# Kernel tuning notes

Hardware: AMD Instinct MI355X
Metric: run time of the kernel (lower is better)

Reference implementation:

```python
import jax, jax.numpy as jnp
import numpy as np

EMBED_DIM = 1024
NUM_HEADS = 16
D_K = EMBED_DIM // NUM_HEADS
MAX_SEQ = 2048
BATCH = 2
SEQ = 2048
ROPE_BASE = 10000.0


def build_rope(seq_len, head_dim, base=ROPE_BASE):
    # standard RoPE: inv_freq over half the head dim, cos/sin of shape [seq, head_dim]
    inv_freq = 1.0 / (base ** (jnp.arange(0, head_dim, 2, dtype=jnp.float32) / head_dim))
    t = jnp.arange(seq_len, dtype=jnp.float32)
    freqs = jnp.einsum('s,d->sd', t, inv_freq)              # [S, D/2]
    emb = jnp.concatenate([freqs, freqs], axis=-1)          # [S, D]
    return jnp.cos(emb), jnp.sin(emb)


def rotate_half(x):
    x1, x2 = jnp.split(x, 2, axis=-1)
    return jnp.concatenate([-x2, x1], axis=-1)


def apply_rope(x, cos, sin):
    # x: [B, H, S, D]; cos/sin: [S, D] -> broadcast over batch & heads
    cos = cos[None, None, :, :]
    sin = sin[None, None, :, :]
    return x * cos + rotate_half(x) * sin


def setup_inputs() -> dict:
    key = jax.random.key(0)
    ks = jax.random.split(key, 9)
    scale = 1.0 / np.sqrt(EMBED_DIM)
    x = jax.random.normal(ks[0], (BATCH, SEQ, EMBED_DIM), dtype=jnp.float32)
    # causal boolean mask, broadcastable to [B, H, S, S]
    mask = jnp.tril(jnp.ones((SEQ, SEQ), dtype=bool))[None, None, :, :]
    cos, sin = build_rope(MAX_SEQ, D_K)
    Wq = jax.random.normal(ks[1], (EMBED_DIM, EMBED_DIM), jnp.float32) * scale
    bq = jnp.zeros((EMBED_DIM,), jnp.float32)
    Wk = jax.random.normal(ks[2], (EMBED_DIM, EMBED_DIM), jnp.float32) * scale
    bk = jnp.zeros((EMBED_DIM,), jnp.float32)
    Wv = jax.random.normal(ks[3], (EMBED_DIM, EMBED_DIM), jnp.float32) * scale
    bv = jnp.zeros((EMBED_DIM,), jnp.float32)
    Wo = jax.random.normal(ks[4], (EMBED_DIM, EMBED_DIM), jnp.float32) * scale
    bo = jnp.zeros((EMBED_DIM,), jnp.float32)
    return {'x': x, 'mask': mask, 'cos': cos, 'sin': sin,
            'Wq': Wq, 'bq': bq, 'Wk': Wk, 'bk': bk, 'Wv': Wv, 'bv': bv,
            'Wo': Wo, 'bo': bo}


def reference(x, mask, cos, sin, Wq, bq, Wk, bk, Wv, bv, Wo, bo):
    B, S, E = x.shape
    H, D = NUM_HEADS, D_K
    # nn.Linear: y = x @ W^T + b
    q = (x @ Wq.T + bq).reshape(B, S, H, D).transpose(0, 2, 1, 3)  # [B,H,S,D]
    k = (x @ Wk.T + bk).reshape(B, S, H, D).transpose(0, 2, 1, 3)
    v = (x @ Wv.T + bv).reshape(B, S, H, D).transpose(0, 2, 1, 3)
    q = apply_rope(q, cos[:S], sin[:S])
    k = apply_rope(k, cos[:S], sin[:S])
    scores = jnp.einsum('bhqd,bhkd->bhqk', q, k) / jnp.sqrt(jnp.float32(D))
    scores = jnp.where(mask, scores, -jnp.inf)
    attn = jax.nn.softmax(scores, axis=-1)
    out = jnp.einsum('bhqk,bhkd->bhqd', attn, v)
    out = out.transpose(0, 2, 1, 3).reshape(B, S, E)
    return out @ Wo.T + bo
```

## Files before the change

kernel.cpp:

```cpp
#include <hip/hip_runtime.h>
#include <hip/hip_bf16.h>
#include <cfloat>
#include <math.h>

#define EMBED 1024
#define NHEADS 16
#define DK 64
#define SEQL 2048
#define BATCH 2
#define NTOK 4096


typedef __bf16 bf16x8 __attribute__((ext_vector_type(8)));
typedef float floatx4 __attribute__((ext_vector_type(4)));

__device__ __forceinline__ unsigned short f2bf(float f) {
    union { __hip_bfloat16 b; unsigned short u; } c;
    c.b = __float2bfloat16(f);
    return c.u;
}

__device__ __forceinline__ void async16(void* lds, const void* g) {
    __builtin_amdgcn_global_load_lds(
        (const __attribute__((address_space(1))) unsigned int*)g,
        (__attribute__((address_space(3))) unsigned int*)lds,
        16, 0, 0);
}

__global__ __launch_bounds__(256) void convert_pack(
    const float* __restrict__ x,  const float* __restrict__ Wq,
    const float* __restrict__ Wk, const float* __restrict__ Wv,
    const float* __restrict__ Wo,
    unsigned short* __restrict__ xb, unsigned short* __restrict__ Wqkv,
    unsigned short* __restrict__ Wob)
{
    const int XG = 1048576, WG = 262144;
    int g = blockIdx.x * 256 + threadIdx.x;
    const float4* s; ushort4* d;
    if (g < XG)               { s = (const float4*)x  + g;                d = (ushort4*)xb   + g; }
    else if (g < XG + WG)     { s = (const float4*)Wq + (g - XG);         d = (ushort4*)Wqkv + (g - XG); }
    else if (g < XG + 2 * WG) { s = (const float4*)Wk + (g - XG - WG);    d = (ushort4*)Wqkv + (g - XG); }
    else if (g < XG + 3 * WG) { s = (const float4*)Wv + (g - XG - 2*WG);  d = (ushort4*)Wqkv + (g - XG); }
    else                      { s = (const float4*)Wo + (g - XG - 3*WG);  d = (ushort4*)Wob  + (g - XG - 3*WG); }
    float4 v = *s;
    *d = (ushort4){f2bf(v.x), f2bf(v.y), f2bf(v.z), f2bf(v.w)};
}

__global__ __launch_bounds__(256) void qkv_gemm(
    const unsigned short* __restrict__ xb, const unsigned short* __restrict__ Wqkv,
    const float* __restrict__ bq, const float* __restrict__ bk, const float* __restrict__ bv,
    const float* __restrict__ cosT, const float* __restrict__ sinT,
    unsigned short* __restrict__ Qg, unsigned short* __restrict__ Kg,
    unsigned short* __restrict__ Vt)
{
    __shared__ __align__(16) unsigned short SM[12288];
    unsigned short* As0 = SM;
    unsigned short* As1 = SM + 4096;
    unsigned short* Bs0 = SM + 8192;
    unsigned short* Bs1 = SM + 10240;

    const int t = threadIdx.x, lane = t & 63, wave = t >> 6;
    const int quad = lane >> 4, lrow = lane & 15;
    const int m0 = blockIdx.y * 128;
    const int n0 = blockIdx.x * 64;
    const int srow = lane >> 2;
    const int scol = (lane & 3) * 8;

    floatx4 acc[2][4];
    #pragma unroll
    for (int i = 0; i < 2; i++)
        #pragma unroll
        for (int j = 0; j < 4; j++) acc[i][j] = (floatx4){0.f,0.f,0.f,0.f};

    for (int k0 = 0; k0 < EMBED; k0 += 64) {
        __syncthreads();
        #pragma unroll
        for (int c = 0; c < 2; c++) {
            const unsigned short* as = xb + (size_t)(m0 + wave * 32 + c * 16 + srow) * EMBED + k0 + scol;
            async16(&As0[wave * 1024 + c * 512], as);
            async16(&As1[wave * 1024 + c * 512], as + 32);
        }
        const unsigned short* bs = Wqkv + (size_t)(n0 + wave * 16 + srow) * EMBED + k0 + scol;
        async16(&Bs0[wave * 512], bs);
        async16(&Bs1[wave * 512], bs + 32);
        __syncthreads();

        #pragma unroll
        for (int ks = 0; ks < 2; ks++) {
            const unsigned short* Ab = ks ? As1 : As0;
            const unsigned short* Bb = ks ? Bs1 : Bs0;
            bf16x8 af[2], bfB[4];
            #pragma unroll
            for (int i = 0; i < 2; i++)
                af[i] = *reinterpret_cast<const bf16x8*>(&Ab[(wave * 32 + i * 16 + lrow) * 32 + quad * 8]);
            #pragma unroll
            for (int j = 0; j < 4; j++)
                bfB[j] = *reinterpret_cast<const bf16x8*>(&Bb[(j * 16 + lrow) * 32 + quad * 8]);
            #pragma unroll
            for (int i = 0; i < 2; i++)
                #pragma unroll
                for (int j = 0; j < 4; j++)
                    acc[i][j] = __builtin_amdgcn_mfma_f32_16x16x32_bf16(af[i], bfB[j], acc[i][j], 0, 0, 0);
        }
    }

    const int mat  = n0 >> 10;
    const int nloc = n0 & 1023;
    const int h    = nloc >> 6;
    const int bb   = m0 >> 11;
    const int s0   = m0 & (SEQL - 1);

    __syncthreads();
    if (mat == 2) {
        unsigned short* T2 = SM;
        #pragma unroll
        for (int j = 0; j < 4; j++) {
            int d = j * 16 + lrow;
            float bvv = bv[nloc + d];
            #pragma unroll
            for (int i = 0; i < 2; i++) {
                int tok = wave * 32 + i * 16 + quad * 4;
                *(ushort4*)&T2[d * 136 + tok] = (ushort4){
                    f2bf(acc[i][j][0] + bvv), f2bf(acc[i][j][1] + bvv),
                    f2bf(acc[i][j][2] + bvv), f2bf(acc[i][j][3] + bvv)};
            }
        }
        __syncthreads();
        int d = t >> 2, tg = (t & 3) * 32;
        unsigned short* dst = Vt + ((size_t)(bb * NHEADS + h) * DK + d) * SEQL + s0 + tg;
        #pragma unroll
        for (int c = 0; c < 32; c += 8)
            *(uint4*)(dst + c) = *(const uint4*)&T2[d * 136 + tg + c];
    } else {
        unsigned short* T = SM;
        const float* bias = (mat == 0) ? bq : bk;
        #pragma unroll
        for (int j = 0; j < 4; j++) {
            int d = j * 16 + lrow;
            float bvv = bias[nloc + d];
            #pragma unroll
            for (int i = 0; i < 2; i++)
                #pragma unroll
                for (int rg = 0; rg < 4; rg++)
                    T[(wave * 32 + i * 16 + quad * 4 + rg) * 72 + d] = f2bf(acc[i][j][rg] + bvv);
        }
        __syncthreads();
        int tok = t >> 1, dh = (t & 1) * 32;
        int s = s0 + tok;
        float sgn = dh ? 1.0f : -1.0f;
        unsigned short* dst = ((mat == 0) ? Qg : Kg)
            + ((size_t)(bb * NHEADS + h) * SEQL + s) * DK + dh;
        #pragma unroll
        for (int c = 0; c < 32; c += 8) {
            bf16x8 own = *reinterpret_cast<const bf16x8*>(&T[tok * 72 + dh + c]);
            bf16x8 par = *reinterpret_cast<const bf16x8*>(&T[tok * 72 + (dh ^ 32) + c]);
            float4 c0 = *(const float4*)(cosT + s * DK + dh + c);
            float4 c1 = *(const float4*)(cosT + s * DK + dh + c + 4);
            float4 s0v = *(const float4*)(sinT + s * DK + dh + c);
            float4 s1v = *(const float4*)(sinT + s * DK + dh + c + 4);
            float cv[8] = {c0.x,c0.y,c0.z,c0.w,c1.x,c1.y,c1.z,c1.w};
            float sv[8] = {s0v.x,s0v.y,s0v.z,s0v.w,s1v.x,s1v.y,s1v.z,s1v.w};
            unsigned short o[8];
            #pragma unroll
            for (int e = 0; e < 8; e++)
                o[e] = f2bf((float)own[e] * cv[e] + sgn * (float)par[e] * sv[e]);
            *(uint4*)(dst + c) = *(const uint4*)o;
        }
    }
}

#define KP 72

__global__ __launch_bounds__(256) void attn_mfma(
    const unsigned short* __restrict__ Qg, const unsigned short* __restrict__ Kg,
    const unsigned short* __restrict__ Vt, unsigned short* __restrict__ CTX)
{
    __shared__ __align__(16) unsigned short Ks[64 * KP];
    __shared__ __align__(16) unsigned short Vs[64 * KP];
    __shared__ __align__(16) unsigned short Ps[64 * KP];

    const int qt = (SEQL / 64 - 1) - blockIdx.x;
    const int h = blockIdx.y, b = blockIdx.z;
    const int t = threadIdx.x;
    const int lane = t & 63, w = t >> 6;
    const int quad = lane >> 4, lrow = lane & 15;
    const int q0 = qt * 64;

    const unsigned short* Qh = Qg + (size_t)(b * NHEADS + h) * SEQL * DK;
    const unsigned short* Kh = Kg + (size_t)(b * NHEADS + h) * SEQL * DK;
    const unsigned short* Vh = Vt + (size_t)(b * NHEADS + h) * DK * SEQL;

    bf16x8 aq[2];
    #pragma unroll
    for (int ks = 0; ks < 2; ks++)
        aq[ks] = *(const bf16x8*)(Qh + (size_t)(q0 + w * 16 + lrow) * DK + quad * 8 + ks * 32);

    floatx4 of[4];
    float l[4] = {0,0,0,0};
    #pragma unroll
    for (int jd = 0; jd < 4; jd++) of[jd] = (floatx4){0,0,0,0};

    unsigned short* Pw = Ps + w * 16 * KP;

    const int r0 = t >> 3, c8 = (t & 7) * 8;
    uint4 pk0, pk1, pv0, pv1;
    auto pref = [&](int k0) {
        pk0 = *(const uint4*)(Kh + (size_t)(k0 + r0) * DK + c8);
        pk1 = *(const uint4*)(Kh + (size_t)(k0 + r0 + 32) * DK + c8);
        pv0 = *(const uint4*)(Vh + (size_t)r0 * SEQL + k0 + c8);
        pv1 = *(const uint4*)(Vh + (size_t)(r0 + 32) * SEQL + k0 + c8);
    };
    pref(0);

    for (int kt = 0; kt <= qt; kt++) {
        const int k0 = kt * 64;
        __syncthreads();
        *(uint4*)&Ks[r0 * KP + c8]        = pk0;
        *(uint4*)&Ks[(r0 + 32) * KP + c8] = pk1;
        *(uint4*)&Vs[r0 * KP + c8]        = pv0;
        *(uint4*)&Vs[(r0 + 32) * KP + c8] = pv1;
        __syncthreads();
        if (kt < qt) pref(k0 + 64);

        floatx4 sc[4];
        #pragma unroll
        for (int j = 0; j < 4; j++) sc[j] = (floatx4){0,0,0,0};
        #pragma unroll
        for (int ks = 0; ks < 2; ks++)
            #pragma unroll
            for (int j = 0; j < 4; j++) {
                bf16x8 kb = *reinterpret_cast<const bf16x8*>(&Ks[(j * 16 + lrow) * KP + quad * 8 + ks * 32]);
                sc[j] = __builtin_amdgcn_mfma_f32_16x16x32_bf16(aq[ks], kb, sc[j], 0, 0, 0);
            }

        const bool diag = (kt == qt);
        #pragma unroll
        for (int rg = 0; rg < 4; rg++) {
            int row = q0 + w * 16 + quad * 4 + rg;
            float lacc = 0.f;
            #pragma unroll
            for (int j = 0; j < 4; j++) {
                float pval = __expf(sc[j][rg] * 0.125f);
                if (diag && (k0 + j * 16 + lrow) > row) pval = 0.f;
                Pw[(quad * 4 + rg) * KP + j * 16 + lrow] = f2bf(pval);
                lacc += pval;
            }
            l[rg] += lacc;
        }
        #pragma unroll
        for (int ks = 0; ks < 2; ks++) {
            bf16x8 pa = *reinterpret_cast<const bf16x8*>(&Pw[lrow * KP + quad * 8 + ks * 32]);
            #pragma unroll
            for (int jd = 0; jd < 4; jd++) {
                bf16x8 vb = *reinterpret_cast<const bf16x8*>(&Vs[(jd * 16 + lrow) * KP + quad * 8 + ks * 32]);
                of[jd] = __builtin_amdgcn_mfma_f32_16x16x32_bf16(pa, vb, of[jd], 0, 0, 0);
            }
        }
    }

    #pragma unroll
    for (int rg = 0; rg < 4; rg++) {
        float lv = l[rg];
        #pragma unroll
        for (int off = 1; off < 16; off <<= 1) lv += __shfl_xor(lv, off);
        float inv = 1.0f / lv;
        int row = q0 + w * 16 + quad * 4 + rg;
        unsigned short* Cr = CTX + ((size_t)(b * NHEADS + h) * SEQL + row) * DK;
        #pragma unroll
        for (int jd = 0; jd < 4; jd++) Cr[jd * 16 + lrow] = f2bf(of[jd][rg] * inv);
    }
}

__global__ __launch_bounds__(256) void o_gemm(
    const unsigned short* __restrict__ Ag,
    const unsigned short* __restrict__ Bg,
    const float* __restrict__ bias, float* __restrict__ C)
{
    __shared__ __align__(16) unsigned short SM[12288];
    unsigned short* As0 = SM;
    unsigned short* As1 = SM + 4096;
    unsigned short* Bs0 = SM + 8192;
    unsigned short* Bs1 = SM + 10240;

    const int t = threadIdx.x, lane = t & 63, wave = t >> 6;
    const int quad = lane >> 4, lrow = lane & 15;
    const int m0 = blockIdx.y * 128, n0 = blockIdx.x * 64;
    const int srow = lane >> 2;
    const int scol = (lane & 3) * 8;

    floatx4 acc[2][4];
    #pragma unroll
    for (int i = 0; i < 2; i++)
        #pragma unroll
        for (int j = 0; j < 4; j++) acc[i][j] = (floatx4){0.f,0.f,0.f,0.f};

    for (int k0 = 0; k0 < EMBED; k0 += 64) {
        const int hh = k0 >> 6;
        __syncthreads();
        #pragma unroll
        for (int c = 0; c < 2; c++) {
            int tok = m0 + wave * 32 + c * 16 + srow;
            const unsigned short* as = Ag
                + ((size_t)((tok >> 11) * NHEADS + hh) * SEQL + (tok & (SEQL - 1))) * DK + scol;
            async16(&As0[wave * 1024 + c * 512], as);
            async16(&As1[wave * 1024 + c * 512], as + 32);
        }
        const unsigned short* bs = Bg + (size_t)(n0 + wave * 16 + srow) * EMBED + k0 + scol;
        async16(&Bs0[wave * 512], bs);
        async16(&Bs1[wave * 512], bs + 32);
        __syncthreads();

        #pragma unroll
        for (int ks = 0; ks < 2; ks++) {
            const unsigned short* Ab = ks ? As1 : As0;
            const unsigned short* Bb = ks ? Bs1 : Bs0;
            bf16x8 af[2], bfB[4];
            #pragma unroll
            for (int i = 0; i < 2; i++)
                af[i] = *reinterpret_cast<const bf16x8*>(&Ab[(wave * 32 + i * 16 + lrow) * 32 + quad * 8]);
            #pragma unroll
            for (int j = 0; j < 4; j++)
                bfB[j] = *reinterpret_cast<const bf16x8*>(&Bb[(j * 16 + lrow) * 32 + quad * 8]);
            #pragma unroll
            for (int i = 0; i < 2; i++)
                #pragma unroll
                for (int j = 0; j < 4; j++)
                    acc[i][j] = __builtin_amdgcn_mfma_f32_16x16x32_bf16(af[i], bfB[j], acc[i][j], 0, 0, 0);
        }
    }

    #pragma unroll
    for (int i = 0; i < 2; i++)
        #pragma unroll
        for (int rg = 0; rg < 4; rg++) {
            int row_g = m0 + wave * 32 + i * 16 + quad * 4 + rg;
            #pragma unroll
            for (int j = 0; j < 4; j++) {
                int col_g = n0 + j * 16 + lrow;
                C[(size_t)row_g * EMBED + col_g] = acc[i][j][rg] + bias[col_g];
            }
        }
}

extern "C" void kernel_launch(void* const* d_in, const int* in_sizes, int n_in,
                              void* d_out, int out_size, void* d_ws, size_t ws_size,
                              hipStream_t stream) {
    const float* x    = (const float*)d_in[0];
    const float* cosT = (const float*)d_in[2];
    const float* sinT = (const float*)d_in[3];
    const float* Wq = (const float*)d_in[4];  const float* bq = (const float*)d_in[5];
    const float* Wk = (const float*)d_in[6];  const float* bk = (const float*)d_in[7];
    const float* Wv = (const float*)d_in[8];  const float* bv = (const float*)d_in[9];
    const float* Wo = (const float*)d_in[10]; const float* bo = (const float*)d_in[11];

    const size_t MB = 1024 * 1024;
    char* ws = (char*)d_ws;
    unsigned short* xb   = (unsigned short*)(ws);
    unsigned short* Wqkv = (unsigned short*)(ws +  8 * MB);
    unsigned short* Wob  = (unsigned short*)(ws + 14 * MB);
    unsigned short* Qg   = (unsigned short*)(ws + 16 * MB);
    unsigned short* Kg   = (unsigned short*)(ws + 24 * MB);
    unsigned short* Vt   = (unsigned short*)(ws + 32 * MB);
    unsigned short* CTXb = (unsigned short*)(ws + 40 * MB);

    convert_pack<<<8192, 256, 0, stream>>>(x, Wq, Wk, Wv, Wo, xb, Wqkv, Wob);

    dim3 qkv_grid(3 * EMBED / 64, NTOK / 128);
    qkv_gemm<<<qkv_grid, 256, 0, stream>>>(xb, Wqkv, bq, bk, bv, cosT, sinT, Qg, Kg, Vt);

    dim3 attn_grid(SEQL / 64, NHEADS, BATCH);
    attn_mfma<<<attn_grid, 256, 0, stream>>>(Qg, Kg, Vt, CTXb);

    dim3 o_grid(EMBED / 64, NTOK / 128);
    o_gemm<<<o_grid, 256, 0, stream>>>(CTXb, Wob, bo, (float*)d_out);
}
```

Measured before the change: 235.9 us.

## Load MFMA operands directly from global memory instead of LDS staging

The QKV GEMM drops its async global-to-LDS staging and barriers. Each wave now loads its A and B MFMA fragments straight from global memory in a k-loop unrolled by 4. The attention kernel likewise removes the shared K/V tiles, their register prefetch and both barriers per tile, reading K and V fragments directly from global memory and relying on L1/L2 to serve the reuse across waves. The P scratch padding shrinks from 72 to 68 elements, which leaves its 16-byte vector reads misaligned and adds exposed global latency with no software prefetch.

```diff
diff --git a/kernel.cpp b/kernel.cpp
--- a/kernel.cpp
+++ b/kernel.cpp
@@ -53,18 +53,12 @@
     unsigned short* __restrict__ Qg, unsigned short* __restrict__ Kg,
     unsigned short* __restrict__ Vt)
 {
-    __shared__ __align__(16) unsigned short SM[12288];
-    unsigned short* As0 = SM;
-    unsigned short* As1 = SM + 4096;
-    unsigned short* Bs0 = SM + 8192;
-    unsigned short* Bs1 = SM + 10240;
+    __shared__ __align__(16) unsigned short SM[9216];
 
     const int t = threadIdx.x, lane = t & 63, wave = t >> 6;
     const int quad = lane >> 4, lrow = lane & 15;
     const int m0 = blockIdx.y * 128;
     const int n0 = blockIdx.x * 64;
-    const int srow = lane >> 2;
-    const int scol = (lane & 3) * 8;
 
     floatx4 acc[2][4];
     #pragma unroll
@@ -72,36 +66,23 @@
         #pragma unroll
         for (int j = 0; j < 4; j++) acc[i][j] = (floatx4){0.f,0.f,0.f,0.f};
 
-    for (int k0 = 0; k0 < EMBED; k0 += 64) {
-        __syncthreads();
-        #pragma unroll
-        for (int c = 0; c < 2; c++) {
-            const unsigned short* as = xb + (size_t)(m0 + wave * 32 + c * 16 + srow) * EMBED + k0 + scol;
-            async16(&As0[wave * 1024 + c * 512], as);
-            async16(&As1[wave * 1024 + c * 512], as + 32);
-        }
-        const unsigned short* bs = Wqkv + (size_t)(n0 + wave * 16 + srow) * EMBED + k0 + scol;
-        async16(&Bs0[wave * 512], bs);
-        async16(&Bs1[wave * 512], bs + 32);
-        __syncthreads();
-
-        #pragma unroll
-        for (int ks = 0; ks < 2; ks++) {
-            const unsigned short* Ab = ks ? As1 : As0;
-            const unsigned short* Bb = ks ? Bs1 : Bs0;
-            bf16x8 af[2], bfB[4];
-            #pragma unroll
-            for (int i = 0; i < 2; i++)
-                af[i] = *reinterpret_cast<const bf16x8*>(&Ab[(wave * 32 + i * 16 + lrow) * 32 + quad * 8]);
+    const unsigned short* A0 = xb   + (size_t)(m0 + wave * 32 + lrow) * EMBED + quad * 8;
+    const unsigned short* B0 = Wqkv + (size_t)(n0 + lrow) * EMBED + quad * 8;
+
+    #pragma unroll 4
+    for (int k0 = 0; k0 < EMBED; k0 += 32) {
+        bf16x8 af[2], bfB[4];
+        #pragma unroll
+        for (int i = 0; i < 2; i++)
+            af[i] = *(const bf16x8*)(A0 + (size_t)i * 16 * EMBED + k0);
+        #pragma unroll
+        for (int j = 0; j < 4; j++)
+            bfB[j] = *(const bf16x8*)(B0 + (size_t)j * 16 * EMBED + k0);
+        #pragma unroll
+        for (int i = 0; i < 2; i++)
             #pragma unroll
             for (int j = 0; j < 4; j++)
-                bfB[j] = *reinterpret_cast<const bf16x8*>(&Bb[(j * 16 + lrow) * 32 + quad * 8]);
-            #pragma unroll
-            for (int i = 0; i < 2; i++)
-                #pragma unroll
-                for (int j = 0; j < 4; j++)
-                    acc[i][j] = __builtin_amdgcn_mfma_f32_16x16x32_bf16(af[i], bfB[j], acc[i][j], 0, 0, 0);
-        }
+                acc[i][j] = __builtin_amdgcn_mfma_f32_16x16x32_bf16(af[i], bfB[j], acc[i][j], 0, 0, 0);
     }
 
     const int mat  = n0 >> 10;
@@ -110,7 +91,6 @@
     const int bb   = m0 >> 11;
     const int s0   = m0 & (SEQL - 1);
 
-    __syncthreads();
     if (mat == 2) {
         unsigned short* T2 = SM;
         #pragma unroll
@@ -169,14 +149,12 @@
     }
 }
 
-#define KP 72
+#define KP 68
 
 __global__ __launch_bounds__(256) void attn_mfma(
     const unsigned short* __restrict__ Qg, const unsigned short* __restrict__ Kg,
     const unsigned short* __restrict__ Vt, unsigned short* __restrict__ CTX)
 {
-    __shared__ __align__(16) unsigned short Ks[64 * KP];
-    __shared__ __align__(16) unsigned short Vs[64 * KP];
     __shared__ __align__(16) unsigned short Ps[64 * KP];
 
     const int qt = (SEQL / 64 - 1) - blockIdx.x;
@@ -202,25 +180,11 @@
 
     unsigned short* Pw = Ps + w * 16 * KP;
 
-    const int r0 = t >> 3, c8 = (t & 7) * 8;
-    uint4 pk0, pk1, pv0, pv1;
-    auto pref = [&](int k0) {
-        pk0 = *(const uint4*)(Kh + (size_t)(k0 + r0) * DK + c8);
-        pk1 = *(const uint4*)(Kh + (size_t)(k0 + r0 + 32) * DK + c8);
-        pv0 = *(const uint4*)(Vh + (size_t)r0 * SEQL + k0 + c8);
-        pv1 = *(const uint4*)(Vh + (size_t)(r0 + 32) * SEQL + k0 + c8);
-    };
-    pref(0);
+    const unsigned short* Kf = Kh + (size_t)lrow * DK + quad * 8;
+    const unsigned short* Vf = Vh + (size_t)lrow * SEQL + quad * 8;
 
     for (int kt = 0; kt <= qt; kt++) {
         const int k0 = kt * 64;
-        __syncthreads();
-        *(uint4*)&Ks[r0 * KP + c8]        = pk0;
-        *(uint4*)&Ks[(r0 + 32) * KP + c8] = pk1;
-        *(uint4*)&Vs[r0 * KP + c8]        = pv0;
-        *(uint4*)&Vs[(r0 + 32) * KP + c8] = pv1;
-        __syncthreads();
-        if (kt < qt) pref(k0 + 64);
 
         floatx4 sc[4];
         #pragma unroll
@@ -229,7 +193,7 @@
         for (int ks = 0; ks < 2; ks++)
             #pragma unroll
             for (int j = 0; j < 4; j++) {
-                bf16x8 kb = *reinterpret_cast<const bf16x8*>(&Ks[(j * 16 + lrow) * KP + quad * 8 + ks * 32]);
+                bf16x8 kb = *(const bf16x8*)(Kf + (size_t)(k0 + j * 16) * DK + ks * 32);
                 sc[j] = __builtin_amdgcn_mfma_f32_16x16x32_bf16(aq[ks], kb, sc[j], 0, 0, 0);
             }
 
@@ -247,12 +211,13 @@
             }
             l[rg] += lacc;
         }
+
         #pragma unroll
         for (int ks = 0; ks < 2; ks++) {
             bf16x8 pa = *reinterpret_cast<const bf16x8*>(&Pw[lrow * KP + quad * 8 + ks * 32]);
             #pragma unroll
             for (int jd = 0; jd < 4; jd++) {
-                bf16x8 vb = *reinterpret_cast<const bf16x8*>(&Vs[(jd * 16 + lrow) * KP + quad * 8 + ks * 32]);
+                bf16x8 vb = *(const bf16x8*)(Vf + (size_t)(jd * 16) * SEQL + k0 + ks * 32);
                 of[jd] = __builtin_amdgcn_mfma_f32_16x16x32_bf16(pa, vb, of[jd], 0, 0, 0);
             }
         }
```

Result: slower. 487.4 us (+106.6%).

## Split attention key range across two blocks and merge with atomics

Applied to the files above, without the earlier changes.

Each causal query tile's key-tile range is split into two halves, each handled by its own block, which doubles the attention grid and evens out per-block work. The partial unnormalized outputs and row sums are accumulated into fp32 buffers with atomicAdd. A separate kernel then normalizes them and converts to bf16. This adds a zeroing kernel, a normalization kernel, extra fp32 global traffic and atomic contention in exchange for better load balance and occupancy.

```diff
diff --git a/kernel.cpp b/kernel.cpp
--- a/kernel.cpp
+++ b/kernel.cpp
@@ -46,6 +46,14 @@
     *d = (ushort4){f2bf(v.x), f2bf(v.y), f2bf(v.z), f2bf(v.w)};
 }
 
+__global__ __launch_bounds__(256) void zero_acc(float4* __restrict__ ctxf,
+                                                float4* __restrict__ lbuf)
+{
+    int g = blockIdx.x * 256 + threadIdx.x;
+    if (g < 1048576) ctxf[g] = (float4){0.f, 0.f, 0.f, 0.f};
+    else             lbuf[g - 1048576] = (float4){0.f, 0.f, 0.f, 0.f};
+}
+
 __global__ __launch_bounds__(256) void qkv_gemm(
     const unsigned short* __restrict__ xb, const unsigned short* __restrict__ Wqkv,
     const float* __restrict__ bq, const float* __restrict__ bk, const float* __restrict__ bv,
@@ -173,18 +181,25 @@
 
 __global__ __launch_bounds__(256) void attn_mfma(
     const unsigned short* __restrict__ Qg, const unsigned short* __restrict__ Kg,
-    const unsigned short* __restrict__ Vt, unsigned short* __restrict__ CTX)
+    const unsigned short* __restrict__ Vt, float* __restrict__ CTXf,
+    float* __restrict__ L)
 {
     __shared__ __align__(16) unsigned short Ks[64 * KP];
     __shared__ __align__(16) unsigned short Vs[64 * KP];
     __shared__ __align__(16) unsigned short Ps[64 * KP];
 
-    const int qt = (SEQL / 64 - 1) - blockIdx.x;
+    const int qt   = (SEQL / 64 - 1) - (blockIdx.x >> 1);
+    const int half = blockIdx.x & 1;
     const int h = blockIdx.y, b = blockIdx.z;
     const int t = threadIdx.x;
     const int lane = t & 63, w = t >> 6;
     const int quad = lane >> 4, lrow = lane & 15;
     const int q0 = qt * 64;
+
+    const int nkt = qt + 1;
+    const int c0  = (nkt + 1) >> 1;
+    const int kt0 = half ? c0 : 0;
+    const int kt1 = half ? nkt : c0;
 
     const unsigned short* Qh = Qg + (size_t)(b * NHEADS + h) * SEQL * DK;
     const unsigned short* Kh = Kg + (size_t)(b * NHEADS + h) * SEQL * DK;
@@ -210,9 +225,9 @@
         pv0 = *(const uint4*)(Vh + (size_t)r0 * SEQL + k0 + c8);
         pv1 = *(const uint4*)(Vh + (size_t)(r0 + 32) * SEQL + k0 + c8);
     };
-    pref(0);
-
-    for (int kt = 0; kt <= qt; kt++) {
+    pref(kt0 * 64);
+
+    for (int kt = kt0; kt < kt1; kt++) {
         const int k0 = kt * 64;
         __syncthreads();
         *(uint4*)&Ks[r0 * KP + c8]        = pk0;
@@ -220,7 +235,7 @@
         *(uint4*)&Vs[r0 * KP + c8]        = pv0;
         *(uint4*)&Vs[(r0 + 32) * KP + c8] = pv1;
         __syncthreads();
-        if (kt < qt) pref(k0 + 64);
+        if (kt + 1 < kt1) pref(k0 + 64);
 
         floatx4 sc[4];
         #pragma unroll
@@ -263,12 +278,25 @@
         float lv = l[rg];
         #pragma unroll
         for (int off = 1; off < 16; off <<= 1) lv += __shfl_xor(lv, off);
-        float inv = 1.0f / lv;
         int row = q0 + w * 16 + quad * 4 + rg;
-        unsigned short* Cr = CTX + ((size_t)(b * NHEADS + h) * SEQL + row) * DK;
-        #pragma unroll
-        for (int jd = 0; jd < 4; jd++) Cr[jd * 16 + lrow] = f2bf(of[jd][rg] * inv);
+        if (lrow == 0) atomicAdd(&L[(size_t)(b * NHEADS + h) * SEQL + row], lv);
+        float* Cr = CTXf + ((size_t)(b * NHEADS + h) * SEQL + row) * DK;
+        #pragma unroll
+        for (int jd = 0; jd < 4; jd++)
+            atomicAdd(&Cr[jd * 16 + lrow], of[jd][rg]);
     }
+}
+
+__global__ __launch_bounds__(256) void attn_norm(
+    const float* __restrict__ ctxf, const float* __restrict__ L,
+    unsigned short* __restrict__ ctxb)
+{
+    int g = blockIdx.x * 256 + threadIdx.x;
+    int row = (g * 4) >> 6;
+    float inv = 1.0f / L[row];
+    float4 v = ((const float4*)ctxf)[g];
+    ((ushort4*)ctxb)[g] = (ushort4){f2bf(v.x * inv), f2bf(v.y * inv),
+                                    f2bf(v.z * inv), f2bf(v.w * inv)};
 }
 
 __global__ __launch_bounds__(256) void o_gemm(
@@ -362,14 +390,20 @@
     unsigned short* Kg   = (unsigned short*)(ws + 24 * MB);
     unsigned short* Vt   = (unsigned short*)(ws + 32 * MB);
     unsigned short* CTXb = (unsigned short*)(ws + 40 * MB);
+    float*          CTXf = (float*)(ws + 48 * MB);
+    float*          Lbuf = (float*)(ws);
 
     convert_pack<<<8192, 256, 0, stream>>>(x, Wq, Wk, Wv, Wo, xb, Wqkv, Wob);
 
     dim3 qkv_grid(3 * EMBED / 64, NTOK / 128);
     qkv_gemm<<<qkv_grid, 256, 0, stream>>>(xb, Wqkv, bq, bk, bv, cosT, sinT, Qg, Kg, Vt);
 
-    dim3 attn_grid(SEQL / 64, NHEADS, BATCH);
-    attn_mfma<<<attn_grid, 256, 0, stream>>>(Qg, Kg, Vt, CTXb);
+    zero_acc<<<4160, 256, 0, stream>>>((float4*)CTXf, (float4*)Lbuf);
+
+    dim3 attn_grid(2 * SEQL / 64, NHEADS, BATCH);
+    attn_mfma<<<attn_grid, 256, 0, stream>>>(Qg, Kg, Vt, CTXf, Lbuf);
+
+    attn_norm<<<4096, 256, 0, stream>>>(CTXf, Lbuf, CTXb);
 
     dim3 o_grid(EMBED / 64, NTOK / 128);
     o_gemm<<<o_grid, 256, 0, stream>>>(CTXb, Wob, bo, (float*)d_out);
```

New measurement: 238.7 us. Within noise of the previous version (+1.2%).

## Replace LDS-direct async loads with register-prefetched, padded LDS tiles in GEMMs

Applied to the files above, without the earlier changes.

Both the QKV and output-projection GEMMs drop the global_load_lds direct-to-LDS copies and the wait they imposed each k-step. Each thread now prefetches the next 64-wide k-tile into registers while MFMAs run on the current tile, then stores it to LDS. The LDS tiles use a padded row stride of 72 to avoid bank conflicts on fragment reads. This costs extra VGPRs and an explicit register-to-LDS store per iteration, and still uses two barriers per step.

```diff
diff --git a/kernel.cpp b/kernel.cpp
--- a/kernel.cpp
+++ b/kernel.cpp
@@ -18,13 +18,6 @@
     union { __hip_bfloat16 b; unsigned short u; } c;
     c.b = __float2bfloat16(f);
     return c.u;
-}
-
-__device__ __forceinline__ void async16(void* lds, const void* g) {
-    __builtin_amdgcn_global_load_lds(
-        (const __attribute__((address_space(1))) unsigned int*)g,
-        (__attribute__((address_space(3))) unsigned int*)lds,
-        16, 0, 0);
 }
 
 __global__ __launch_bounds__(256) void convert_pack(
@@ -46,6 +39,8 @@
     *d = (ushort4){f2bf(v.x), f2bf(v.y), f2bf(v.z), f2bf(v.w)};
 }
 
+#define PA 72
+
 __global__ __launch_bounds__(256) void qkv_gemm(
     const unsigned short* __restrict__ xb, const unsigned short* __restrict__ Wqkv,
     const float* __restrict__ bq, const float* __restrict__ bk, const float* __restrict__ bv,
@@ -53,18 +48,20 @@
     unsigned short* __restrict__ Qg, unsigned short* __restrict__ Kg,
     unsigned short* __restrict__ Vt)
 {
-    __shared__ __align__(16) unsigned short SM[12288];
-    unsigned short* As0 = SM;
-    unsigned short* As1 = SM + 4096;
-    unsigned short* Bs0 = SM + 8192;
-    unsigned short* Bs1 = SM + 10240;
+    __shared__ __align__(16) unsigned short SM[128 * PA + 64 * PA];
+    unsigned short* As = SM;
+    unsigned short* Bs = SM + 128 * PA;
 
     const int t = threadIdx.x, lane = t & 63, wave = t >> 6;
     const int quad = lane >> 4, lrow = lane & 15;
     const int m0 = blockIdx.y * 128;
     const int n0 = blockIdx.x * 64;
-    const int srow = lane >> 2;
-    const int scol = (lane & 3) * 8;
+
+    const int ar = t >> 1, ac = (t & 1) * 32;
+    const int br = t >> 2, bc = (t & 3) * 16;
+
+    const unsigned short* Agp = xb   + (size_t)(m0 + ar) * EMBED + ac;
+    const unsigned short* Bgp = Wqkv + (size_t)(n0 + br) * EMBED + bc;
 
     floatx4 acc[2][4];
     #pragma unroll
@@ -72,30 +69,33 @@
         #pragma unroll
         for (int j = 0; j < 4; j++) acc[i][j] = (floatx4){0.f,0.f,0.f,0.f};
 
-    for (int k0 = 0; k0 < EMBED; k0 += 64) {
-        __syncthreads();
-        #pragma unroll
-        for (int c = 0; c < 2; c++) {
-            const unsigned short* as = xb + (size_t)(m0 + wave * 32 + c * 16 + srow) * EMBED + k0 + scol;
-            async16(&As0[wave * 1024 + c * 512], as);
-            async16(&As1[wave * 1024 + c * 512], as + 32);
-        }
-        const unsigned short* bs = Wqkv + (size_t)(n0 + wave * 16 + srow) * EMBED + k0 + scol;
-        async16(&Bs0[wave * 512], bs);
-        async16(&Bs1[wave * 512], bs + 32);
-        __syncthreads();
+    uint4 pa[4], pb[2];
+    auto load = [&](int k0) {
+        #pragma unroll
+        for (int u = 0; u < 4; u++) pa[u] = *(const uint4*)(Agp + k0 + 8 * u);
+        #pragma unroll
+        for (int u = 0; u < 2; u++) pb[u] = *(const uint4*)(Bgp + k0 + 8 * u);
+    };
+
+    load(0);
+    for (int it = 0; it < 16; it++) {
+        __syncthreads();
+        #pragma unroll
+        for (int u = 0; u < 4; u++) *(uint4*)&As[ar * PA + ac + 8 * u] = pa[u];
+        #pragma unroll
+        for (int u = 0; u < 2; u++) *(uint4*)&Bs[br * PA + bc + 8 * u] = pb[u];
+        __syncthreads();
+        if (it < 15) load((it + 1) * 64);
 
         #pragma unroll
         for (int ks = 0; ks < 2; ks++) {
-            const unsigned short* Ab = ks ? As1 : As0;
-            const unsigned short* Bb = ks ? Bs1 : Bs0;
             bf16x8 af[2], bfB[4];
             #pragma unroll
             for (int i = 0; i < 2; i++)
-                af[i] = *reinterpret_cast<const bf16x8*>(&Ab[(wave * 32 + i * 16 + lrow) * 32 + quad * 8]);
+                af[i] = *reinterpret_cast<const bf16x8*>(&As[(wave * 32 + i * 16 + lrow) * PA + quad * 8 + ks * 32]);
             #pragma unroll
             for (int j = 0; j < 4; j++)
-                bfB[j] = *reinterpret_cast<const bf16x8*>(&Bb[(j * 16 + lrow) * 32 + quad * 8]);
+                bfB[j] = *reinterpret_cast<const bf16x8*>(&Bs[(j * 16 + lrow) * PA + quad * 8 + ks * 32]);
             #pragma unroll
             for (int i = 0; i < 2; i++)
                 #pragma unroll
@@ -276,17 +276,20 @@
     const unsigned short* __restrict__ Bg,
     const float* __restrict__ bias, float* __restrict__ C)
 {
-    __shared__ __align__(16) unsigned short SM[12288];
-    unsigned short* As0 = SM;
-    unsigned short* As1 = SM + 4096;
-    unsigned short* Bs0 = SM + 8192;
-    unsigned short* Bs1 = SM + 10240;
+    __shared__ __align__(16) unsigned short SM[128 * PA + 64 * PA];
+    unsigned short* As = SM;
+    unsigned short* Bs = SM + 128 * PA;
 
     const int t = threadIdx.x, lane = t & 63, wave = t >> 6;
     const int quad = lane >> 4, lrow = lane & 15;
     const int m0 = blockIdx.y * 128, n0 = blockIdx.x * 64;
-    const int srow = lane >> 2;
-    const int scol = (lane & 3) * 8;
+
+    const int ar = t >> 1, ac = (t & 1) * 32;
+    const int br = t >> 2, bc = (t & 3) * 16;
+
+    const int tokA = m0 + ar;
+    const size_t arowbase = ((size_t)(tokA >> 11) * NHEADS) * SEQL + (tokA & (SEQL - 1));
+    const unsigned short* Bgp = Bg + (size_t)(n0 + br) * EMBED + bc;
 
     floatx4 acc[2][4];
     #pragma unroll
@@ -294,33 +297,34 @@
         #pragma unroll
         for (int j = 0; j < 4; j++) acc[i][j] = (floatx4){0.f,0.f,0.f,0.f};
 
-    for (int k0 = 0; k0 < EMBED; k0 += 64) {
-        const int hh = k0 >> 6;
-        __syncthreads();
-        #pragma unroll
-        for (int c = 0; c < 2; c++) {
-            int tok = m0 + wave * 32 + c * 16 + srow;
-            const unsigned short* as = Ag
-                + ((size_t)((tok >> 11) * NHEADS + hh) * SEQL + (tok & (SEQL - 1))) * DK + scol;
-            async16(&As0[wave * 1024 + c * 512], as);
-            async16(&As1[wave * 1024 + c * 512], as + 32);
-        }
-        const unsigned short* bs = Bg + (size_t)(n0 + wave * 16 + srow) * EMBED + k0 + scol;
-        async16(&Bs0[wave * 512], bs);
-        async16(&Bs1[wave * 512], bs + 32);
-        __syncthreads();
+    uint4 pa[4], pb[2];
+    auto load = [&](int k0) {
+        const unsigned short* a = Ag + (arowbase + (size_t)(k0 >> 6) * SEQL) * DK + ac;
+        #pragma unroll
+        for (int u = 0; u < 4; u++) pa[u] = *(const uint4*)(a + 8 * u);
+        #pragma unroll
+        for (int u = 0; u < 2; u++) pb[u] = *(const uint4*)(Bgp + k0 + 8 * u);
+    };
+
+    load(0);
+    for (int it = 0; it < 16; it++) {
+        __syncthreads();
+        #pragma unroll
+        for (int u = 0; u < 4; u++) *(uint4*)&As[ar * PA + ac + 8 * u] = pa[u];
+        #pragma unroll
+        for (int u = 0; u < 2; u++) *(uint4*)&Bs[br * PA + bc + 8 * u] = pb[u];
+        __syncthreads();
+        if (it < 15) load((it + 1) * 64);
 
         #pragma unroll
         for (int ks = 0; ks < 2; ks++) {
-            const unsigned short* Ab = ks ? As1 : As0;
-            const unsigned short* Bb = ks ? Bs1 : Bs0;
             bf16x8 af[2], bfB[4];
             #pragma unroll
             for (int i = 0; i < 2; i++)
-                af[i] = *reinterpret_cast<const bf16x8*>(&Ab[(wave * 32 + i * 16 + lrow) * 32 + quad * 8]);
+                af[i] = *reinterpret_cast<const bf16x8*>(&As[(wave * 32 + i * 16 + lrow) * PA + quad * 8 + ks * 32]);
             #pragma unroll
             for (int j = 0; j < 4; j++)
-                bfB[j] = *reinterpret_cast<const bf16x8*>(&Bb[(j * 16 + lrow) * 32 + quad * 8]);
+                bfB[j] = *reinterpret_cast<const bf16x8*>(&Bs[(j * 16 + lrow) * PA + quad * 8 + ks * 32]);
             #pragma unroll
             for (int i = 0; i < 2; i++)
                 #pragma unroll
```

New measurement: 404.0 us. 1.71x slower.
